# Kernel optimization log

Hardware: AMD Instinct MI355X
Metric: run time of the kernel (lower is better)

The kernel has to match this reference:

```python
import jax, jax.numpy as jnp
import numpy as np

B, T, D_IN, D_OUT, H = 2, 2048, 512, 512, 8
DK = D_OUT // H


def setup_inputs() -> dict:
    key = jax.random.key(0)
    ks = jax.random.split(key, 11)
    s = 0.02
    return {
        "q": jax.random.normal(ks[0], (B, T, D_IN), jnp.float32),
        "k": jax.random.normal(ks[1], (B, T, D_IN), jnp.float32),
        "v": jax.random.normal(ks[2], (B, T, D_IN), jnp.float32),
        "Wq": jax.random.normal(ks[3], (D_OUT, D_IN), jnp.float32) * s,
        "bq": jnp.zeros((D_OUT,), jnp.float32),
        "Wk": jax.random.normal(ks[4], (D_OUT, D_IN), jnp.float32) * s,
        "bk": jnp.zeros((D_OUT,), jnp.float32),
        "Wv": jax.random.normal(ks[5], (D_OUT, D_IN), jnp.float32) * s,
        "bv": jnp.zeros((D_OUT,), jnp.float32),
        "Wo": jax.random.normal(ks[6], (D_IN, D_OUT), jnp.float32) * s,
        "bo": jnp.zeros((D_IN,), jnp.float32),
    }


def reference(q, k, v, Wq, bq, Wk, bk, Wv, bv, Wo, bo):
    def proj(x, W, b):
        # [B,T,D_in] @ [D_in,D_out] -> [B,H,T,DK]
        return (x @ W.T + b).reshape(B, T, H, DK).transpose(0, 2, 1, 3)

    qh = proj(q, Wq, bq)
    kh = proj(k, Wk, bk)
    vh = proj(v, Wv, bv)
    # NOTE: original code applies NO 1/sqrt(d_k) scaling
    scores = jnp.einsum("bhqd,bhkd->bhqk", qh, kh)  # [B,H,T,T]
    p = jax.nn.softmax(scores, axis=-1)
    # mean-threshold sparsification: keep entries strictly above row mean
    p = jnp.where(p > p.mean(axis=-1, keepdims=True), p, jnp.zeros_like(p))
    out = jnp.einsum("bhqk,bhkd->bhqd", p, vh)  # [B,H,T,DK]
    concat = out.transpose(0, 2, 1, 3).reshape(B, T, D_OUT)
    return concat @ Wo.T + bo  # [B,T,D_IN]
```

## Files before the change

kernel.cpp:

```cpp
#include <hip/hip_runtime.h>

constexpr int B_   = 2;
constexpr int T_   = 2048;
constexpr int DIN  = 512;
constexpr int DOUT = 512;
constexpr int H_   = 8;
constexpr int DK_  = 64;

constexpr float LOG2E = 1.44269504088896340736f;

typedef float    f32x16  __attribute__((ext_vector_type(16)));
typedef short    short8v __attribute__((ext_vector_type(8)));
typedef __bf16   bf16x8  __attribute__((ext_vector_type(8)));

__device__ inline f32x16 mfma3216(short8v a, short8v b, f32x16 c) {
    return __builtin_amdgcn_mfma_f32_32x32x16_bf16(
        __builtin_bit_cast(bf16x8, a), __builtin_bit_cast(bf16x8, b), c, 0, 0, 0);
}

__device__ inline unsigned short bf16c(float f) {
    return __builtin_bit_cast(unsigned short, (__bf16)f);
}
__device__ inline float bf2f(unsigned short u) {
    return (float)__builtin_bit_cast(__bf16, u);
}
__device__ inline unsigned pk2(float lo, float hi) {
    return (unsigned)bf16c(lo) | ((unsigned)bf16c(hi) << 16);
}
__device__ __forceinline__ void pl32swap(unsigned &x, unsigned &y) {
    asm("v_permlane32_swap_b32 %0, %1" : "+v"(x), "+v"(y));
}

__global__ __launch_bounds__(256) void wconvert_kernel(
    const float* __restrict__ Wq, const float* __restrict__ Wk,
    const float* __restrict__ Wv, const float* __restrict__ Wo,
    unsigned short* __restrict__ Wh, unsigned short* __restrict__ Wl)
{
    const int b = blockIdx.x, t = threadIdx.x;
    const int wi = b >> 6;
    const float* src = wi == 0 ? Wq : (wi == 1 ? Wk : (wi == 2 ? Wv : Wo));
    unsigned short* hi = Wh + (size_t)wi * 262144;
    unsigned short* lo = Wl + (size_t)wi * 262144;
    const float scl = (wi == 0) ? LOG2E : 1.0f;
    const size_t off = (size_t)(b & 63) * 4096;
#pragma unroll
    for (int c = 0; c < 4; ++c) {
        const size_t idx = off + (size_t)c * 1024 + (size_t)t * 4;
        float4 x = *(const float4*)&src[idx];
        x.x *= scl; x.y *= scl; x.z *= scl; x.w *= scl;
        ushort4 h;
        h.x = bf16c(x.x); h.y = bf16c(x.y); h.z = bf16c(x.z); h.w = bf16c(x.w);
        *(ushort4*)&hi[idx] = h;
        ushort4 l2;
        l2.x = bf16c(x.x - bf2f(h.x));
        l2.y = bf16c(x.y - bf2f(h.y));
        l2.z = bf16c(x.z - bf2f(h.z));
        l2.w = bf16c(x.w - bf2f(h.w));
        *(ushort4*)&lo[idx] = l2;
    }
}

template<int MODE>
__device__ __forceinline__ void store_c(unsigned short* __restrict__ outb,
                                        float* __restrict__ outf,
                                        int m, int n, float v)
{
    if constexpr (MODE == 0) {
        outf[(size_t)m * DOUT + n] = v;
    } else {
        const int bb = m >> 11, t = m & (T_ - 1);
        const int hh = n >> 6,  d = n & (DK_ - 1);
        const size_t bh = (size_t)bb * H_ + hh;
        if constexpr (MODE == 1) {
            outb[(bh * T_ + t) * DK_ + d] = bf16c(v);
        } else if constexpr (MODE == 3) {
            const int kt = t >> 5, l31 = t & 31;
            const int c = d >> 4, khi = (d >> 3) & 1, e = d & 7;
            outb[(bh * 64 + kt) * 2048 + (c * 2 + khi) * 256 + l31 * 8 + e] = bf16c(v);
        } else {
            const int kt = t >> 5, kgrp = (t >> 4) & 1, khi = (t >> 3) & 1, e = t & 7;
            const int dblk = d >> 5, l31 = d & 31;
            outb[(bh * 64 + kt) * 2048 + ((kgrp * 2 + dblk) * 2 + khi) * 256 + l31 * 8 + e] = bf16c(v);
        }
    }
}

template<int MODE, bool AF32, int BN>
__device__ inline void gemm_body(
    const void* __restrict__ Av, const unsigned short* __restrict__ Bhp,
    const unsigned short* __restrict__ Blp, const float* __restrict__ bias,
    float bscale,
    unsigned short* __restrict__ outb, float* __restrict__ outf)
{
    __shared__ unsigned short As[128 * 32];
    __shared__ unsigned short Bsh[BN * 32];
    __shared__ unsigned short Bsl[BN * 32];

    const int tid = threadIdx.x;
    const int m0 = blockIdx.y * 128, n0 = blockIdx.x * BN;
    const int lane31 = tid & 31, hi8 = (tid & 63) >> 5;
    const int wv = tid >> 6, wm = wv >> 1, wn = wv & 1;

    const int r_  = tid >> 2, pos_ = tid & 3;
    const int r2_ = r_ + 64;
    const int sw_  = pos_ ^ ((r_  >> 1) & 3);
    const int sw2_ = pos_ ^ ((r2_ >> 1) & 3);

    short8v a0r, a1r, bh0r, bl0r, bh1r, bl1r;

    auto gload = [&](int kb) {
        const int k0 = kb * 32;
        if constexpr (AF32) {
            const float* Af = (const float*)Av;
            {
                const float4 f0 = *(const float4*)&Af[(size_t)(m0 + r_) * DIN + k0 + pos_ * 8];
                const float4 f1 = *(const float4*)&Af[(size_t)(m0 + r_) * DIN + k0 + pos_ * 8 + 4];
                union { unsigned w[4]; short8v v; } u;
                u.w[0] = pk2(f0.x, f0.y); u.w[1] = pk2(f0.z, f0.w);
                u.w[2] = pk2(f1.x, f1.y); u.w[3] = pk2(f1.z, f1.w);
                a0r = u.v;
            }
            {
                const float4 f0 = *(const float4*)&Af[(size_t)(m0 + r2_) * DIN + k0 + pos_ * 8];
                const float4 f1 = *(const float4*)&Af[(size_t)(m0 + r2_) * DIN + k0 + pos_ * 8 + 4];
                union { unsigned w[4]; short8v v; } u;
                u.w[0] = pk2(f0.x, f0.y); u.w[1] = pk2(f0.z, f0.w);
                u.w[2] = pk2(f1.x, f1.y); u.w[3] = pk2(f1.z, f1.w);
                a1r = u.v;
            }
        } else {
            const unsigned short* Ab = (const unsigned short*)Av;
            a0r = *(const short8v*)&Ab[(size_t)(m0 + r_)  * DIN + k0 + pos_ * 8];
            a1r = *(const short8v*)&Ab[(size_t)(m0 + r2_) * DIN + k0 + pos_ * 8];
        }
        bh0r = *(const short8v*)&Bhp[(size_t)(n0 + r_) * DIN + k0 + pos_ * 8];
        bl0r = *(const short8v*)&Blp[(size_t)(n0 + r_) * DIN + k0 + pos_ * 8];
        if constexpr (BN == 128) {
            bh1r = *(const short8v*)&Bhp[(size_t)(n0 + r2_) * DIN + k0 + pos_ * 8];
            bl1r = *(const short8v*)&Blp[(size_t)(n0 + r2_) * DIN + k0 + pos_ * 8];
        }
    };
    auto swrite = [&]() {
        *(short8v*)((char*)As + r_  * 64 + sw_  * 16) = a0r;
        *(short8v*)((char*)As + r2_ * 64 + sw2_ * 16) = a1r;
        *(short8v*)((char*)Bsh + r_ * 64 + sw_ * 16) = bh0r;
        *(short8v*)((char*)Bsl + r_ * 64 + sw_ * 16) = bl0r;
        if constexpr (BN == 128) {
            *(short8v*)((char*)Bsh + r2_ * 64 + sw2_ * 16) = bh1r;
            *(short8v*)((char*)Bsl + r2_ * 64 + sw2_ * 16) = bl1r;
        }
    };

    f32x16 acc00 = {}, acc01 = {}, acc10 = {}, acc11 = {};

    gload(0);
    for (int kb = 0; kb < 16; ++kb) {
        swrite();
        __syncthreads();
        if (kb < 15) gload(kb + 1);
#pragma unroll
        for (int ks = 0; ks < 2; ++ks) {
            const int pos = ks * 2 + hi8;
            short8v a0, a1;
            { const int r = wm * 64 + lane31;
              a0 = *(const short8v*)((char*)As + r * 64 + ((pos ^ ((r >> 1) & 3)) << 4)); }
            { const int r = wm * 64 + 32 + lane31;
              a1 = *(const short8v*)((char*)As + r * 64 + ((pos ^ ((r >> 1) & 3)) << 4)); }
            if constexpr (BN == 64) {
                short8v b0h, b0l;
                { const int r = wn * 32 + lane31;
                  b0h = *(const short8v*)((char*)Bsh + r * 64 + ((pos ^ ((r >> 1) & 3)) << 4));
                  b0l = *(const short8v*)((char*)Bsl + r * 64 + ((pos ^ ((r >> 1) & 3)) << 4)); }
                acc00 = mfma3216(a0, b0h, acc00);
                acc00 = mfma3216(a0, b0l, acc00);
                acc10 = mfma3216(a1, b0h, acc10);
                acc10 = mfma3216(a1, b0l, acc10);
            } else {
                short8v b0h, b0l, b1h, b1l;
                { const int r = wn * 64 + lane31;
                  b0h = *(const short8v*)((char*)Bsh + r * 64 + ((pos ^ ((r >> 1) & 3)) << 4));
                  b0l = *(const short8v*)((char*)Bsl + r * 64 + ((pos ^ ((r >> 1) & 3)) << 4)); }
                { const int r = wn * 64 + 32 + lane31;
                  b1h = *(const short8v*)((char*)Bsh + r * 64 + ((pos ^ ((r >> 1) & 3)) << 4));
                  b1l = *(const short8v*)((char*)Bsl + r * 64 + ((pos ^ ((r >> 1) & 3)) << 4)); }
                acc00 = mfma3216(a0, b0h, acc00);
                acc00 = mfma3216(a0, b0l, acc00);
                acc01 = mfma3216(a0, b1h, acc01);
                acc01 = mfma3216(a0, b1l, acc01);
                acc10 = mfma3216(a1, b0h, acc10);
                acc10 = mfma3216(a1, b0l, acc10);
                acc11 = mfma3216(a1, b1h, acc11);
                acc11 = mfma3216(a1, b1l, acc11);
            }
        }
        __syncthreads();
    }

    const int nb = n0 + wn * (BN / 2) + lane31;
#pragma unroll
    for (int r = 0; r < 16; ++r) {
        const int row = (r & 3) + 8 * (r >> 2) + 4 * hi8;
        store_c<MODE>(outb, outf, m0 + wm * 64 + row,      nb, acc00[r] + bias[nb] * bscale);
        store_c<MODE>(outb, outf, m0 + wm * 64 + 32 + row, nb, acc10[r] + bias[nb] * bscale);
        if constexpr (BN == 128) {
            store_c<MODE>(outb, outf, m0 + wm * 64 + row,      nb + 32, acc01[r] + bias[nb + 32] * bscale);
            store_c<MODE>(outb, outf, m0 + wm * 64 + 32 + row, nb + 32, acc11[r] + bias[nb + 32] * bscale);
        }
    }
}

__global__ __launch_bounds__(256) void qkv_gemm(
    const float* __restrict__ q, const float* __restrict__ k, const float* __restrict__ v,
    const unsigned short* __restrict__ Wh, const unsigned short* __restrict__ Wl,
    const float* __restrict__ bq, const float* __restrict__ bk, const float* __restrict__ bv,
    unsigned short* __restrict__ Qh, unsigned short* __restrict__ Kf,
    unsigned short* __restrict__ Vf)
{
    const int z = blockIdx.z;
    if (z == 0)      gemm_body<1, true, 128>(q, Wh,          Wl,          bq, LOG2E, Qh, nullptr);
    else if (z == 1) gemm_body<3, true, 128>(k, Wh + 262144, Wl + 262144, bk, 1.0f,  Kf, nullptr);
    else             gemm_body<4, true, 128>(v, Wh + 524288, Wl + 524288, bv, 1.0f,  Vf, nullptr);
}

__global__ __launch_bounds__(256) void out_gemm(
    const unsigned short* __restrict__ A,
    const unsigned short* __restrict__ Bh, const unsigned short* __restrict__ Bl,
    const float* __restrict__ bias, float* __restrict__ out)
{
    gemm_body<0, false, 64>(A, Bh, Bl, bias, 1.0f, nullptr, out);
}

__global__ __launch_bounds__(512) void attn_kernel(
    const unsigned short* __restrict__ Qh, const unsigned short* __restrict__ Kf,
    const unsigned short* __restrict__ Vf, unsigned short* __restrict__ concat)
{
    __shared__ float lds_l[8][32];
    __shared__ float lds_out[4][32][64];

    const int bid = blockIdx.x;
    const int xcd = bid & 7;
    const int j   = bid >> 3;
    const int bh  = 2 * xcd + (j >> 6);
    const int qt  = j & 63;

    const int tid    = threadIdx.x;
    const int w      = tid >> 6;
    const int l      = tid & 63;
    const int lane31 = l & 31;
    const int hi     = l >> 5;

    const int q0 = qt * 32;
    const unsigned short* Qb = Qh + ((size_t)bh * T_ + q0) * DK_;

    short8v qf[4];
#pragma unroll
    for (int c = 0; c < 4; ++c)
        qf[c] = *(const short8v*)(Qb + (size_t)lane31 * DK_ + c * 16 + hi * 8);

    const unsigned short* Kw = Kf + ((size_t)bh * 64 + w * 8) * 2048 + hi * 256 + lane31 * 8;
    const unsigned short* Vw = Vf + ((size_t)bh * 64 + w * 8) * 2048 + hi * 256 + lane31 * 8;

    float ls0 = 0.f, ls1 = 0.f, ls2 = 0.f, ls3 = 0.f;
    for (int kt = 0; kt < 8; ++kt) {
        const unsigned short* Kt = Kw + kt * 2048;
        short8v kf[4];
#pragma unroll
        for (int c = 0; c < 4; ++c)
            kf[c] = *(const short8v*)(Kt + c * 512);
        f32x16 acc = {};
        __builtin_amdgcn_s_setprio(1);
#pragma unroll
        for (int c = 0; c < 4; ++c)
            acc = mfma3216(kf[c], qf[c], acc);
        __builtin_amdgcn_s_setprio(0);
#pragma unroll
        for (int r = 0; r < 16; r += 4) {
            ls0 += __builtin_amdgcn_exp2f(acc[r + 0]);
            ls1 += __builtin_amdgcn_exp2f(acc[r + 1]);
            ls2 += __builtin_amdgcn_exp2f(acc[r + 2]);
            ls3 += __builtin_amdgcn_exp2f(acc[r + 3]);
        }
    }
    float lsum = (ls0 + ls1) + (ls2 + ls3);
    lsum += __shfl_xor(lsum, 32);
    if (l < 32) lds_l[w][l] = lsum;
    __syncthreads();
    float ltot = 0.f;
#pragma unroll
    for (int i = 0; i < 8; ++i) ltot += lds_l[i][lane31];
    const float thr = ltot * (1.0f / 2048.0f);
    const float inv = 1.0f / ltot;

    f32x16 o0 = {}, o1 = {};
    for (int kt = 0; kt < 8; ++kt) {
        const unsigned short* Kt = Kw + kt * 2048;
        short8v kf[4];
#pragma unroll
        for (int c = 0; c < 4; ++c)
            kf[c] = *(const short8v*)(Kt + c * 512);
        f32x16 acc = {};
        __builtin_amdgcn_s_setprio(1);
#pragma unroll
        for (int c = 0; c < 4; ++c)
            acc = mfma3216(kf[c], qf[c], acc);
        __builtin_amdgcn_s_setprio(0);

        float p[16];
#pragma unroll
        for (int r = 0; r < 16; ++r) {
            const float e = __builtin_amdgcn_exp2f(acc[r]);
            p[r] = (e > thr) ? e : 0.f;
        }

        short8v pa[2];
#pragma unroll
        for (int h = 0; h < 2; ++h) {
            unsigned a  = pk2(p[8 * h + 0], p[8 * h + 1]);
            unsigned b2 = pk2(p[8 * h + 2], p[8 * h + 3]);
            unsigned c2 = pk2(p[8 * h + 4], p[8 * h + 5]);
            unsigned d2 = pk2(p[8 * h + 6], p[8 * h + 7]);
            pl32swap(a, c2);
            pl32swap(b2, d2);
            union { unsigned w2[4]; short8v v8; } u;
            u.w2[0] = a; u.w2[1] = b2; u.w2[2] = c2; u.w2[3] = d2;
            pa[h] = u.v8;
        }

        const unsigned short* Vt_ = Vw + kt * 2048;
        short8v vf0 = *(const short8v*)(Vt_);
        short8v vf1 = *(const short8v*)(Vt_ + 512);
        short8v vf2 = *(const short8v*)(Vt_ + 1024);
        short8v vf3 = *(const short8v*)(Vt_ + 1536);
        __builtin_amdgcn_s_setprio(1);
        o0 = mfma3216(pa[0], vf0, o0);
        o1 = mfma3216(pa[0], vf1, o1);
        o0 = mfma3216(pa[1], vf2, o0);
        o1 = mfma3216(pa[1], vf3, o1);
        __builtin_amdgcn_s_setprio(0);
    }

    if (w >= 4) {
#pragma unroll
        for (int r = 0; r < 16; ++r) {
            const int row = (r & 3) + 8 * (r >> 2) + 4 * hi;
            lds_out[w - 4][row][lane31]      = o0[r];
            lds_out[w - 4][row][32 + lane31] = o1[r];
        }
    }
    __syncthreads();
    if (w < 4) {
#pragma unroll
        for (int r = 0; r < 16; ++r) {
            const int row = (r & 3) + 8 * (r >> 2) + 4 * hi;
            o0[r] += lds_out[w][row][lane31];
            o1[r] += lds_out[w][row][32 + lane31];
        }
    }
    __syncthreads();
    if (w >= 1 && w < 4) {
#pragma unroll
        for (int r = 0; r < 16; ++r) {
            const int row = (r & 3) + 8 * (r >> 2) + 4 * hi;
            lds_out[w - 1][row][lane31]      = o0[r];
            lds_out[w - 1][row][32 + lane31] = o1[r];
        }
    }
    __syncthreads();
    if (w == 0) {
        const int b = bh >> 3, h = bh & 7;
        unsigned short* Cb = concat + ((size_t)b * T_ + q0) * DOUT + h * DK_;
#pragma unroll
        for (int r = 0; r < 16; ++r) {
            const int row = (r & 3) + 8 * (r >> 2) + 4 * hi;
            const float iv = __shfl(inv, row);
            const float v0 = o0[r] + lds_out[0][row][lane31]
                           + lds_out[1][row][lane31] + lds_out[2][row][lane31];
            const float v1 = o1[r] + lds_out[0][row][32 + lane31]
                           + lds_out[1][row][32 + lane31] + lds_out[2][row][32 + lane31];
            Cb[(size_t)row * DOUT + lane31]      = bf16c(v0 * iv);
            Cb[(size_t)row * DOUT + 32 + lane31] = bf16c(v1 * iv);
        }
    }
}

extern "C" void kernel_launch(void* const* d_in, const int* in_sizes, int n_in,
                              void* d_out, int out_size, void* d_ws, size_t ws_size,
                              hipStream_t stream)
{
    const float* q  = (const float*)d_in[0];
    const float* k  = (const float*)d_in[1];
    const float* v  = (const float*)d_in[2];
    const float* Wq = (const float*)d_in[3];
    const float* bq = (const float*)d_in[4];
    const float* Wk = (const float*)d_in[5];
    const float* bk = (const float*)d_in[6];
    const float* Wv = (const float*)d_in[7];
    const float* bv = (const float*)d_in[8];
    const float* Wo = (const float*)d_in[9];
    const float* bo = (const float*)d_in[10];
    float* out = (float*)d_out;

    constexpr size_t M2 = 2097152;
    unsigned short* ws     = (unsigned short*)d_ws;
    unsigned short* Qh     = ws;
    unsigned short* Kf     = ws + 1 * M2;
    unsigned short* Vf     = ws + 2 * M2;
    unsigned short* concat = ws + 3 * M2;
    unsigned short* Wh     = ws + 4 * M2;
    unsigned short* Wl     = ws + 4 * M2 + 1048576;

    wconvert_kernel<<<256, 256, 0, stream>>>(Wq, Wk, Wv, Wo, Wh, Wl);
    qkv_gemm<<<dim3(4, 32, 3), 256, 0, stream>>>(q, k, v, Wh, Wl, bq, bk, bv, Qh, Kf, Vf);
    attn_kernel<<<dim3(1024), 512, 0, stream>>>(Qh, Kf, Vf, concat);
    out_gemm<<<dim3(8, 32), 256, 0, stream>>>(concat, Wh + 786432, Wl + 786432, bo, out);
}
```

Baseline: 88.81 us.

## Process two 32-row query tiles per attention block to reuse K/V loads

Each attention block now handles 64 query rows (two 32-row sub-tiles) instead of 32, so every K and V fragment loaded from global memory feeds twice as many MFMAs. The grid is halved to 512 blocks, and the cross-wave output reduction runs twice per block. The intent is to cut K/V memory traffic per unit of work. In exchange it raises register pressure (four output accumulators, two Q fragment sets) and reduces the number of blocks available to fill the GPU.

```diff
diff --git a/kernel.cpp b/kernel.cpp
--- a/kernel.cpp
+++ b/kernel.cpp
@@ -234,14 +234,14 @@
     const unsigned short* __restrict__ Qh, const unsigned short* __restrict__ Kf,
     const unsigned short* __restrict__ Vf, unsigned short* __restrict__ concat)
 {
-    __shared__ float lds_l[8][32];
+    __shared__ float lds_l[8][2][32];
     __shared__ float lds_out[4][32][64];
 
     const int bid = blockIdx.x;
     const int xcd = bid & 7;
     const int j   = bid >> 3;
-    const int bh  = 2 * xcd + (j >> 6);
-    const int qt  = j & 63;
+    const int bh  = 2 * xcd + (j >> 5);
+    const int qt  = j & 31;
 
     const int tid    = threadIdx.x;
     const int w      = tid >> 6;
@@ -249,137 +249,207 @@
     const int lane31 = l & 31;
     const int hi     = l >> 5;
 
-    const int q0 = qt * 32;
-    const unsigned short* Qb = Qh + ((size_t)bh * T_ + q0) * DK_;
-
-    short8v qf[4];
-#pragma unroll
-    for (int c = 0; c < 4; ++c)
-        qf[c] = *(const short8v*)(Qb + (size_t)lane31 * DK_ + c * 16 + hi * 8);
+    const int q0 = qt * 64;
+    const unsigned short* Qb0 = Qh + ((size_t)bh * T_ + q0) * DK_;
+    const unsigned short* Qb1 = Qb0 + (size_t)32 * DK_;
+
+    short8v qf0[4], qf1[4];
+#pragma unroll
+    for (int c = 0; c < 4; ++c) {
+        qf0[c] = *(const short8v*)(Qb0 + (size_t)lane31 * DK_ + c * 16 + hi * 8);
+        qf1[c] = *(const short8v*)(Qb1 + (size_t)lane31 * DK_ + c * 16 + hi * 8);
+    }
 
     const unsigned short* Kw = Kf + ((size_t)bh * 64 + w * 8) * 2048 + hi * 256 + lane31 * 8;
     const unsigned short* Vw = Vf + ((size_t)bh * 64 + w * 8) * 2048 + hi * 256 + lane31 * 8;
 
-    float ls0 = 0.f, ls1 = 0.f, ls2 = 0.f, ls3 = 0.f;
+    float a_ls0 = 0.f, a_ls1 = 0.f, a_ls2 = 0.f, a_ls3 = 0.f;
+    float b_ls0 = 0.f, b_ls1 = 0.f, b_ls2 = 0.f, b_ls3 = 0.f;
     for (int kt = 0; kt < 8; ++kt) {
         const unsigned short* Kt = Kw + kt * 2048;
         short8v kf[4];
 #pragma unroll
         for (int c = 0; c < 4; ++c)
             kf[c] = *(const short8v*)(Kt + c * 512);
-        f32x16 acc = {};
-        __builtin_amdgcn_s_setprio(1);
-#pragma unroll
-        for (int c = 0; c < 4; ++c)
-            acc = mfma3216(kf[c], qf[c], acc);
-        __builtin_amdgcn_s_setprio(0);
-#pragma unroll
-        for (int r = 0; r < 16; r += 4) {
-            ls0 += __builtin_amdgcn_exp2f(acc[r + 0]);
-            ls1 += __builtin_amdgcn_exp2f(acc[r + 1]);
-            ls2 += __builtin_amdgcn_exp2f(acc[r + 2]);
-            ls3 += __builtin_amdgcn_exp2f(acc[r + 3]);
-        }
-    }
-    float lsum = (ls0 + ls1) + (ls2 + ls3);
-    lsum += __shfl_xor(lsum, 32);
-    if (l < 32) lds_l[w][l] = lsum;
+        {
+            f32x16 acc = {};
+            __builtin_amdgcn_s_setprio(1);
+#pragma unroll
+            for (int c = 0; c < 4; ++c)
+                acc = mfma3216(kf[c], qf0[c], acc);
+            __builtin_amdgcn_s_setprio(0);
+#pragma unroll
+            for (int r = 0; r < 16; r += 4) {
+                a_ls0 += __builtin_amdgcn_exp2f(acc[r + 0]);
+                a_ls1 += __builtin_amdgcn_exp2f(acc[r + 1]);
+                a_ls2 += __builtin_amdgcn_exp2f(acc[r + 2]);
+                a_ls3 += __builtin_amdgcn_exp2f(acc[r + 3]);
+            }
+        }
+        {
+            f32x16 acc = {};
+            __builtin_amdgcn_s_setprio(1);
+#pragma unroll
+            for (int c = 0; c < 4; ++c)
+                acc = mfma3216(kf[c], qf1[c], acc);
+            __builtin_amdgcn_s_setprio(0);
+#pragma unroll
+            for (int r = 0; r < 16; r += 4) {
+                b_ls0 += __builtin_amdgcn_exp2f(acc[r + 0]);
+                b_ls1 += __builtin_amdgcn_exp2f(acc[r + 1]);
+                b_ls2 += __builtin_amdgcn_exp2f(acc[r + 2]);
+                b_ls3 += __builtin_amdgcn_exp2f(acc[r + 3]);
+            }
+        }
+    }
+    float lsum0 = (a_ls0 + a_ls1) + (a_ls2 + a_ls3);
+    float lsum1 = (b_ls0 + b_ls1) + (b_ls2 + b_ls3);
+    lsum0 += __shfl_xor(lsum0, 32);
+    lsum1 += __shfl_xor(lsum1, 32);
+    if (l < 32) { lds_l[w][0][l] = lsum0; lds_l[w][1][l] = lsum1; }
     __syncthreads();
-    float ltot = 0.f;
-#pragma unroll
-    for (int i = 0; i < 8; ++i) ltot += lds_l[i][lane31];
-    const float thr = ltot * (1.0f / 2048.0f);
-    const float inv = 1.0f / ltot;
-
-    f32x16 o0 = {}, o1 = {};
+    float ltot0 = 0.f, ltot1 = 0.f;
+#pragma unroll
+    for (int i = 0; i < 8; ++i) { ltot0 += lds_l[i][0][lane31]; ltot1 += lds_l[i][1][lane31]; }
+    const float thr0 = ltot0 * (1.0f / 2048.0f);
+    const float thr1 = ltot1 * (1.0f / 2048.0f);
+    const float inv0 = 1.0f / ltot0;
+    const float inv1 = 1.0f / ltot1;
+
+    f32x16 o00 = {}, o01 = {}, o10 = {}, o11 = {};
     for (int kt = 0; kt < 8; ++kt) {
         const unsigned short* Kt = Kw + kt * 2048;
         short8v kf[4];
 #pragma unroll
         for (int c = 0; c < 4; ++c)
             kf[c] = *(const short8v*)(Kt + c * 512);
-        f32x16 acc = {};
-        __builtin_amdgcn_s_setprio(1);
-#pragma unroll
-        for (int c = 0; c < 4; ++c)
-            acc = mfma3216(kf[c], qf[c], acc);
-        __builtin_amdgcn_s_setprio(0);
-
-        float p[16];
-#pragma unroll
-        for (int r = 0; r < 16; ++r) {
-            const float e = __builtin_amdgcn_exp2f(acc[r]);
-            p[r] = (e > thr) ? e : 0.f;
-        }
-
-        short8v pa[2];
-#pragma unroll
-        for (int h = 0; h < 2; ++h) {
-            unsigned a  = pk2(p[8 * h + 0], p[8 * h + 1]);
-            unsigned b2 = pk2(p[8 * h + 2], p[8 * h + 3]);
-            unsigned c2 = pk2(p[8 * h + 4], p[8 * h + 5]);
-            unsigned d2 = pk2(p[8 * h + 6], p[8 * h + 7]);
-            pl32swap(a, c2);
-            pl32swap(b2, d2);
-            union { unsigned w2[4]; short8v v8; } u;
-            u.w2[0] = a; u.w2[1] = b2; u.w2[2] = c2; u.w2[3] = d2;
-            pa[h] = u.v8;
+
+        short8v pa0[2], pa1[2];
+        {
+            f32x16 acc = {};
+            __builtin_amdgcn_s_setprio(1);
+#pragma unroll
+            for (int c = 0; c < 4; ++c)
+                acc = mfma3216(kf[c], qf0[c], acc);
+            __builtin_amdgcn_s_setprio(0);
+            float p[16];
+#pragma unroll
+            for (int r = 0; r < 16; ++r) {
+                const float e = __builtin_amdgcn_exp2f(acc[r]);
+                p[r] = (e > thr0) ? e : 0.f;
+            }
+#pragma unroll
+            for (int h = 0; h < 2; ++h) {
+                unsigned a  = pk2(p[8 * h + 0], p[8 * h + 1]);
+                unsigned b2 = pk2(p[8 * h + 2], p[8 * h + 3]);
+                unsigned c2 = pk2(p[8 * h + 4], p[8 * h + 5]);
+                unsigned d2 = pk2(p[8 * h + 6], p[8 * h + 7]);
+                pl32swap(a, c2);
+                pl32swap(b2, d2);
+                union { unsigned w2[4]; short8v v8; } u;
+                u.w2[0] = a; u.w2[1] = b2; u.w2[2] = c2; u.w2[3] = d2;
+                pa0[h] = u.v8;
+            }
+        }
+        {
+            f32x16 acc = {};
+            __builtin_amdgcn_s_setprio(1);
+#pragma unroll
+            for (int c = 0; c < 4; ++c)
+                acc = mfma3216(kf[c], qf1[c], acc);
+            __builtin_amdgcn_s_setprio(0);
+            float p[16];
+#pragma unroll
+            for (int r = 0; r < 16; ++r) {
+                const float e = __builtin_amdgcn_exp2f(acc[r]);
+                p[r] = (e > thr1) ? e : 0.f;
+            }
+#pragma unroll
+            for (int h = 0; h < 2; ++h) {
+                unsigned a  = pk2(p[8 * h + 0], p[8 * h + 1]);
+                unsigned b2 = pk2(p[8 * h + 2], p[8 * h + 3]);
+                unsigned c2 = pk2(p[8 * h + 4], p[8 * h + 5]);
+                unsigned d2 = pk2(p[8 * h + 6], p[8 * h + 7]);
+                pl32swap(a, c2);
+                pl32swap(b2, d2);
+                union { unsigned w2[4]; short8v v8; } u;
+                u.w2[0] = a; u.w2[1] = b2; u.w2[2] = c2; u.w2[3] = d2;
+                pa1[h] = u.v8;
+            }
         }
 
         const unsigned short* Vt_ = Vw + kt * 2048;
-        short8v vf0 = *(const short8v*)(Vt_);
-        short8v vf1 = *(const short8v*)(Vt_ + 512);
-        short8v vf2 = *(const short8v*)(Vt_ + 1024);
-        short8v vf3 = *(const short8v*)(Vt_ + 1536);
-        __builtin_amdgcn_s_setprio(1);
-        o0 = mfma3216(pa[0], vf0, o0);
-        o1 = mfma3216(pa[0], vf1, o1);
-        o0 = mfma3216(pa[1], vf2, o0);
-        o1 = mfma3216(pa[1], vf3, o1);
-        __builtin_amdgcn_s_setprio(0);
-    }
-
-    if (w >= 4) {
-#pragma unroll
-        for (int r = 0; r < 16; ++r) {
-            const int row = (r & 3) + 8 * (r >> 2) + 4 * hi;
-            lds_out[w - 4][row][lane31]      = o0[r];
-            lds_out[w - 4][row][32 + lane31] = o1[r];
-        }
-    }
-    __syncthreads();
-    if (w < 4) {
-#pragma unroll
-        for (int r = 0; r < 16; ++r) {
-            const int row = (r & 3) + 8 * (r >> 2) + 4 * hi;
-            o0[r] += lds_out[w][row][lane31];
-            o1[r] += lds_out[w][row][32 + lane31];
-        }
-    }
-    __syncthreads();
-    if (w >= 1 && w < 4) {
-#pragma unroll
-        for (int r = 0; r < 16; ++r) {
-            const int row = (r & 3) + 8 * (r >> 2) + 4 * hi;
-            lds_out[w - 1][row][lane31]      = o0[r];
-            lds_out[w - 1][row][32 + lane31] = o1[r];
-        }
-    }
-    __syncthreads();
-    if (w == 0) {
-        const int b = bh >> 3, h = bh & 7;
-        unsigned short* Cb = concat + ((size_t)b * T_ + q0) * DOUT + h * DK_;
-#pragma unroll
-        for (int r = 0; r < 16; ++r) {
-            const int row = (r & 3) + 8 * (r >> 2) + 4 * hi;
-            const float iv = __shfl(inv, row);
-            const float v0 = o0[r] + lds_out[0][row][lane31]
-                           + lds_out[1][row][lane31] + lds_out[2][row][lane31];
-            const float v1 = o1[r] + lds_out[0][row][32 + lane31]
-                           + lds_out[1][row][32 + lane31] + lds_out[2][row][32 + lane31];
-            Cb[(size_t)row * DOUT + lane31]      = bf16c(v0 * iv);
-            Cb[(size_t)row * DOUT + 32 + lane31] = bf16c(v1 * iv);
-        }
+        {
+            short8v vf0 = *(const short8v*)(Vt_);
+            short8v vf1 = *(const short8v*)(Vt_ + 512);
+            __builtin_amdgcn_s_setprio(1);
+            o00 = mfma3216(pa0[0], vf0, o00);
+            o01 = mfma3216(pa0[0], vf1, o01);
+            o10 = mfma3216(pa1[0], vf0, o10);
+            o11 = mfma3216(pa1[0], vf1, o11);
+            __builtin_amdgcn_s_setprio(0);
+        }
+        {
+            short8v vf2 = *(const short8v*)(Vt_ + 1024);
+            short8v vf3 = *(const short8v*)(Vt_ + 1536);
+            __builtin_amdgcn_s_setprio(1);
+            o00 = mfma3216(pa0[1], vf2, o00);
+            o01 = mfma3216(pa0[1], vf3, o01);
+            o10 = mfma3216(pa1[1], vf2, o10);
+            o11 = mfma3216(pa1[1], vf3, o11);
+            __builtin_amdgcn_s_setprio(0);
+        }
+    }
+
+    const int b = bh >> 3, h = bh & 7;
+#pragma unroll
+    for (int s = 0; s < 2; ++s) {
+        f32x16& o0 = s ? o10 : o00;
+        f32x16& o1 = s ? o11 : o01;
+        const float inv = s ? inv1 : inv0;
+
+        if (w >= 4) {
+#pragma unroll
+            for (int r = 0; r < 16; ++r) {
+                const int row = (r & 3) + 8 * (r >> 2) + 4 * hi;
+                lds_out[w - 4][row][lane31]      = o0[r];
+                lds_out[w - 4][row][32 + lane31] = o1[r];
+            }
+        }
+        __syncthreads();
+        if (w < 4) {
+#pragma unroll
+            for (int r = 0; r < 16; ++r) {
+                const int row = (r & 3) + 8 * (r >> 2) + 4 * hi;
+                o0[r] += lds_out[w][row][lane31];
+                o1[r] += lds_out[w][row][32 + lane31];
+            }
+        }
+        __syncthreads();
+        if (w >= 1 && w < 4) {
+#pragma unroll
+            for (int r = 0; r < 16; ++r) {
+                const int row = (r & 3) + 8 * (r >> 2) + 4 * hi;
+                lds_out[w - 1][row][lane31]      = o0[r];
+                lds_out[w - 1][row][32 + lane31] = o1[r];
+            }
+        }
+        __syncthreads();
+        if (w == 0) {
+            unsigned short* Cb = concat + ((size_t)b * T_ + q0 + s * 32) * DOUT + h * DK_;
+#pragma unroll
+            for (int r = 0; r < 16; ++r) {
+                const int row = (r & 3) + 8 * (r >> 2) + 4 * hi;
+                const float iv = __shfl(inv, row);
+                const float v0 = o0[r] + lds_out[0][row][lane31]
+                               + lds_out[1][row][lane31] + lds_out[2][row][lane31];
+                const float v1 = o1[r] + lds_out[0][row][32 + lane31]
+                               + lds_out[1][row][32 + lane31] + lds_out[2][row][32 + lane31];
+                Cb[(size_t)row * DOUT + lane31]      = bf16c(v0 * iv);
+                Cb[(size_t)row * DOUT + 32 + lane31] = bf16c(v1 * iv);
+            }
+        }
+        __syncthreads();
     }
 }
 
@@ -411,6 +481,6 @@
 
     wconvert_kernel<<<256, 256, 0, stream>>>(Wq, Wk, Wv, Wo, Wh, Wl);
     qkv_gemm<<<dim3(4, 32, 3), 256, 0, stream>>>(q, k, v, Wh, Wl, bq, bk, bv, Qh, Kf, Vf);
-    attn_kernel<<<dim3(1024), 512, 0, stream>>>(Qh, Kf, Vf, concat);
+    attn_kernel<<<dim3(512), 512, 0, stream>>>(Qh, Kf, Vf, concat);
     out_gemm<<<dim3(8, 32), 256, 0, stream>>>(concat, Wh + 786432, Wl + 786432, bo, out);
 }
```

Result: no change. 89.83 us (+1.1%).
